# Kernel tuning notes

Measured on AMD Instinct MI355X. Metric: run time of the kernel, lower is better.

The kernel has to match this reference:

```python
import jax, jax.numpy as jnp
import numpy as np

K = 20
EPS_BN = 1e-5

def knn_idx(x, k):
    # x: [B,N,C] -> k nearest neighbor indices [B,N,k] (self included, as in DGCNN)
    sq = jnp.sum(x * x, axis=-1)                       # [B,N]
    inner = jnp.einsum('bnc,bmc->bnm', x, x)           # [B,N,N]
    neg_dist = 2.0 * inner - sq[:, :, None] - sq[:, None, :]
    _, idx = jax.lax.top_k(neg_dist, k)
    return jax.lax.stop_gradient(idx)

def edge_feat(x, idx):
    # x: [B,N,C], idx: [B,N,k] -> [B,N,k,2C] = cat([x_j - x_i, x_i])
    nbr = jax.vmap(lambda xb, ib: xb[ib])(x, idx)      # [B,N,k,C]
    ctr = jnp.broadcast_to(x[:, :, None, :], nbr.shape)
    return jnp.concatenate([nbr - ctr, ctr], axis=-1)

def edge_conv(x, W, g, b, k):
    e = edge_feat(x, knn_idx(x, k))                    # dynamic kNN graph per layer
    h = jnp.einsum('bnkc,cd->bnkd', e, W)              # 1x1 conv2d
    h = h * (g / jnp.sqrt(1.0 + EPS_BN)) + b           # BN eval (mean=0, var=1)
    return jnp.max(jax.nn.leaky_relu(h, 0.2), axis=2)  # max over neighbors -> [B,N,d]

def layer_norm(x, g, b):
    m = jnp.mean(x, axis=-1, keepdims=True)
    v = jnp.var(x, axis=-1, keepdims=True)
    return (x - m) * jax.lax.rsqrt(v + 1e-5) * g + b

def setup_inputs():
    key = jax.random.key(0)
    B, N = 2, 4096
    ks = jax.random.split(key, 16)
    w = lambda i, shape: jax.random.normal(ks[i], shape, jnp.float32) * 0.05
    ones = lambda d: jnp.ones((d,), jnp.float32)
    zeros = lambda d: jnp.zeros((d,), jnp.float32)
    return dict(
        xyz=jax.random.normal(ks[0], (N, 3), jnp.float32),
        scale=jax.random.normal(ks[1], (N, 3), jnp.float32),
        rot=jax.random.normal(ks[2], (N, 4), jnp.float32),
        opacity=jax.random.normal(ks[3], (N, 1), jnp.float32),
        color=jax.random.normal(ks[4], (N, 3), jnp.float32),
        pose=jax.random.normal(ks[5], (B, 75), jnp.float32),
        lbs_weights=jax.random.normal(ks[6], (N, 24), jnp.float32),
        Wc1=w(7, (226, 64)), g1=ones(64), b1=zeros(64),
        Wc2=w(8, (128, 64)), g2=ones(64), b2=zeros(64),
        Wc3=w(9, (128, 128)), g3=ones(128), b3=zeros(128),
        Wc4=w(10, (256, 256)), g4=ones(256), b4=zeros(256),
        Wc5=w(11, (512, 128)), g5=ones(128), b5=zeros(128),
        Wo1=w(12, (128, 128)), bo1=zeros(128), lg1=ones(128), lb1=zeros(128),
        Wo2=w(13, (128, 128)), bo2=zeros(128), lg2=ones(128), lb2=zeros(128),
        Wo3=w(14, (128, 38)), bo3=zeros(38),
    )

def reference(xyz, scale, rot, opacity, color, pose, lbs_weights,
              Wc1, g1, b1, Wc2, g2, b2, Wc3, g3, b3, Wc4, g4, b4, Wc5, g5, b5,
              Wo1, bo1, lg1, lb1, Wo2, bo2, lg2, lb2, Wo3, bo3):
    B, N = pose.shape[0], xyz.shape[0]
    gfeat = jnp.concatenate([xyz, scale, rot, opacity, color], axis=-1)   # [N,14]
    feats = jnp.concatenate([
        jnp.broadcast_to(gfeat[None], (B, N, gfeat.shape[-1])),
        jnp.broadcast_to(lbs_weights[None], (B, N, lbs_weights.shape[-1])),
        jnp.broadcast_to(pose[:, None, :], (B, N, pose.shape[-1])),
    ], axis=-1)                                                            # [B,N,113]
    # DGCNN graph encoder (dynamic kNN EdgeConv stack)
    x1 = edge_conv(feats, Wc1, g1, b1, K)   # [B,N,64]
    x2 = edge_conv(x1, Wc2, g2, b2, K)      # [B,N,64]
    x3 = edge_conv(x2, Wc3, g3, b3, K)      # [B,N,128]
    x4 = edge_conv(x3, Wc4, g4, b4, K)      # [B,N,256]
    cat = jnp.concatenate([x1, x2, x3, x4], axis=-1)                      # [B,N,512]
    gf = jax.nn.leaky_relu(
        jnp.einsum('bnc,cd->bnd', cat, Wc5) * (g5 / jnp.sqrt(1.0 + EPS_BN)) + b5, 0.2)
    # offset predictor MLP
    h = jax.nn.leaky_relu(layer_norm(gf @ Wo1 + bo1, lg1, lb1), 0.2)
    h = jax.nn.leaky_relu(layer_norm(h @ Wo2 + bo2, lg2, lb2), 0.2)
    off = h @ Wo3 + bo3                                                   # [B,N,38]
    # residual add of gaussian offsets (first 14 dims), lbs offsets raw (last 24)
    out = jnp.concatenate([gfeat[None] + off[..., :14], off[..., 14:]], axis=-1)
    return out                                                            # [B,N,38]
```

## Files before the change

kernel.cpp:

```cpp
#include <hip/hip_runtime.h>
#include <math.h>

#define KNN 20
#define BN_INV 0.9999950000374997f

__device__ __forceinline__ unsigned f2o(float f){
    unsigned u = __float_as_uint(f);
    return (u >> 31) ? ~u : (u | 0x80000000u);
}
__device__ __forceinline__ float o2f(unsigned u){
    return __uint_as_float((u >> 31) ? (u & 0x7fffffffu) : ~u);
}
__device__ __forceinline__ float leaky(float v){ return v > 0.f ? v : 0.2f * v; }

__global__ __launch_bounds__(128) void build_feats_kernel(
    const float* __restrict__ xyz, const float* __restrict__ scale,
    const float* __restrict__ rot, const float* __restrict__ opac,
    const float* __restrict__ color, const float* __restrict__ pose,
    const float* __restrict__ lbs, float* __restrict__ feats,
    float* __restrict__ sqout, int N)
{
    __shared__ float sred[2];
    int row = blockIdx.x;
    int b = row / N, n = row % N;
    int c = threadIdx.x;
    float v = 0.f;
    if      (c <   3) v = xyz  [n*3 + c];
    else if (c <   6) v = scale[n*3 + c-3];
    else if (c <  10) v = rot  [n*4 + c-6];
    else if (c <  11) v = opac [n];
    else if (c <  14) v = color[n*3 + c-11];
    else if (c <  38) v = lbs  [n*24 + c-14];
    else if (c < 113) v = pose [b*75 + c-38];
    if (c < 116) feats[(long)row*116 + c] = v;
    float ss = v * v;
    #pragma unroll
    for (int off = 32; off; off >>= 1) ss += __shfl_xor(ss, off);
    if ((c & 63) == 0) sred[c >> 6] = ss;
    __syncthreads();
    if (c == 0) sqout[row] = sred[0] + sred[1];
}


template<int C>
__global__ __launch_bounds__(256) void dist_gemm_kernel(
    const float* __restrict__ x, int N, int CP, float* __restrict__ G)
{
    __shared__ __align__(16) float smem[9216];
    float (*xi)[36] = (float(*)[36])smem;
    float (*xj)[36] = (float(*)[36])(smem + 128*36);

    const int q = blockIdx.x;
    int bjt = (int)((sqrtf(8.f*(float)q + 1.f) - 1.f) * 0.5f);
    while ((bjt+1)*(bjt+2)/2 <= q) ++bjt;
    while (bjt*(bjt+1)/2 > q) --bjt;
    const int bit = q - bjt*(bjt+1)/2;
    const int bi = bit * 128;
    const int bj = bjt * 128;

    const int b  = blockIdx.z;
    const int t  = threadIdx.x;
    const int tx = t & 15, ty = t >> 4;
    const int CP4 = CP / 4;
    const long base = (long)b * N;
    const float4* xp = (const float4*)x;

    float acc[8][8] = {};

    for (int c0 = 0; c0 < C; c0 += 32){
        const int KC  = (C - c0 < 32) ? (C - c0) : 32;
        const int KC4 = KC >> 2;
        __syncthreads();
        if (KC4 == 8){
            for (int f = t; f < 128 * 8; f += 256){
                int r = f >> 3, c4 = f & 7;
                *(float4*)&xi[r][c4 * 4] = xp[(base + bi + r) * CP4 + (c0 >> 2) + c4];
                *(float4*)&xj[r][c4 * 4] = xp[(base + bj + r) * CP4 + (c0 >> 2) + c4];
            }
        } else {
            for (int f = t; f < 128 * KC4; f += 256){
                int r = f / KC4, c4 = f - r * KC4;
                *(float4*)&xi[r][c4 * 4] = xp[(base + bi + r) * CP4 + (c0 >> 2) + c4];
                *(float4*)&xj[r][c4 * 4] = xp[(base + bj + r) * CP4 + (c0 >> 2) + c4];
            }
        }
        __syncthreads();
        for (int c = 0; c < KC; c += 4){
            float4 A[8], Bv[8];
            #pragma unroll
            for (int ii = 0; ii < 8; ++ii) A[ii]  = *(const float4*)&xi[ty + 16*ii][c];
            #pragma unroll
            for (int jj = 0; jj < 8; ++jj) Bv[jj] = *(const float4*)&xj[tx + 16*jj][c];
            #pragma unroll
            for (int ii = 0; ii < 8; ++ii)
                #pragma unroll
                for (int jj = 0; jj < 8; ++jj){
                    acc[ii][jj] = fmaf(A[ii].x, Bv[jj].x, acc[ii][jj]);
                    acc[ii][jj] = fmaf(A[ii].y, Bv[jj].y, acc[ii][jj]);
                    acc[ii][jj] = fmaf(A[ii].z, Bv[jj].z, acc[ii][jj]);
                    acc[ii][jj] = fmaf(A[ii].w, Bv[jj].w, acc[ii][jj]);
                }
        }
    }

    #pragma unroll
    for (int ii = 0; ii < 8; ++ii){
        long rbase = (base + bi + ty + 16*ii) * N + bj;
        #pragma unroll
        for (int jj = 0; jj < 8; ++jj)
            G[rbase + tx + 16*jj] = acc[ii][jj];
    }

    if (bi != bj){
        float (*tr)[132] = (float(*)[132])smem;
        #pragma unroll
        for (int h = 0; h < 2; ++h){
            __syncthreads();
            #pragma unroll
            for (int ii = 0; ii < 8; ++ii)
                #pragma unroll
                for (int jj = 4*h; jj < 4*h + 4; ++jj)
                    tr[tx + 16*(jj - 4*h)][ty + 16*ii] = acc[ii][jj];
            __syncthreads();
            const int cc = (t & 31) * 4;
            const int r0 = t >> 5;
            #pragma unroll
            for (int f = 0; f < 8; ++f){
                int r = r0 + 8 * f;
                *(float4*)&G[(base + bj + 64*h + r) * N + bi + cc] = *(const float4*)&tr[r][cc];
            }
        }
    }
}

#define TCAP 256
__global__ __launch_bounds__(256) void topk_kernel(
    const float* __restrict__ G, const float* __restrict__ sq,
    int N, int* __restrict__ idx_out)
{
    __shared__ unsigned smax[256];
    __shared__ unsigned cand_u[TCAP];
    __shared__ int      cand_j[TCAP];
    __shared__ unsigned cand_cnt;
    __shared__ unsigned sTu;

    const int row = blockIdx.x;
    const int b   = row >> 12;
    const int t   = threadIdx.x;
    const float4* g4  = (const float4*)(G  + (long)row * 4096);
    const float4* sq4 = (const float4*)(sq + (long)b   * 4096);

    unsigned u[16];
    #pragma unroll
    for (int qq = 0; qq < 4; ++qq){
        int v4 = t + 256 * qq;
        float4 gg = g4[v4];
        float4 ss = sq4[v4];
        u[4*qq+0] = f2o(fmaf(2.f, gg.x, -ss.x));
        u[4*qq+1] = f2o(fmaf(2.f, gg.y, -ss.y));
        u[4*qq+2] = f2o(fmaf(2.f, gg.z, -ss.z));
        u[4*qq+3] = f2o(fmaf(2.f, gg.w, -ss.w));
    }

    unsigned mu = u[0];
    #pragma unroll
    for (int q = 1; q < 16; ++q) mu = u[q] > mu ? u[q] : mu;
    smax[t] = mu;
    if (t == 0) cand_cnt = 0;
    __syncthreads();

    int rank = 0;
    for (int k = 0; k < 256; ++k){
        unsigned ou = smax[k];
        rank += (ou > mu) || (ou == mu && k < t);
    }
    if (rank == KNN - 1) sTu = mu;
    __syncthreads();
    const unsigned Tu = sTu;

    #pragma unroll
    for (int qq = 0; qq < 4; ++qq)
        #pragma unroll
        for (int m = 0; m < 4; ++m){
            int q = 4*qq + m;
            if (u[q] >= Tu){
                unsigned p = atomicAdd(&cand_cnt, 1u);
                if (p < TCAP){ cand_u[p] = u[q]; cand_j[p] = 4*(t + 256*qq) + m; }
            }
        }
    __syncthreads();
    const int cc = (int)cand_cnt;

    if (cc <= TCAP){
        if (t < cc){
            unsigned cu = cand_u[t]; int cj = cand_j[t];
            int r = 0;
            for (int k = 0; k < cc; ++k){
                unsigned ou = cand_u[k];
                r += (ou > cu) || (ou == cu && cand_j[k] < cj);
            }
            if (r < KNN) idx_out[(long)row * KNN + r] = cj;
        }
    } else {
        __shared__ unsigned rv[4]; __shared__ int ri[4]; __shared__ int gj_;
        unsigned lv = 0u; int lj = 0x7fffffff;
        #pragma unroll
        for (int q = 0; q < 16; ++q)
            if (u[q] > lv){ lv = u[q]; lj = 4*(t + 256*(q>>2)) + (q&3); }
        for (int it = 0; it < KNN; ++it){
            unsigned bv = lv; int bj = lj;
            #pragma unroll
            for (int off = 32; off; off >>= 1){
                unsigned ov = __shfl_xor(bv, off);
                int      oj = __shfl_xor(bj, off);
                if (ov > bv || (ov == bv && oj < bj)){ bv = ov; bj = oj; }
            }
            if ((t & 63) == 0){ rv[t >> 6] = bv; ri[t >> 6] = bj; }
            __syncthreads();
            if (t == 0){
                unsigned fv = rv[0]; int fj = ri[0];
                #pragma unroll
                for (int w = 1; w < 4; ++w)
                    if (rv[w] > fv || (rv[w] == fv && ri[w] < fj)){ fv = rv[w]; fj = ri[w]; }
                gj_ = fj;
                idx_out[(long)row * KNN + it] = fj;
            }
            __syncthreads();
            int fj = gj_;
            if (fj >= 0 && ((fj >> 2) & 255) == t){
                u[((fj >> 10) << 2) | (fj & 3)] = 0u;
                lv = 0u; lj = 0x7fffffff;
                #pragma unroll
                for (int q = 0; q < 16; ++q)
                    if (u[q] > lv){ lv = u[q]; lj = 4*(t + 256*(q>>2)) + (q&3); }
            }
            __syncthreads();
        }
    }
}


__device__ __forceinline__ void wcat_emit(const float* __restrict__ W, int C, int D,
                                          int i, float* __restrict__ dst)
{
    int TWOD = 2 * D;
    int c = i / TWOD, n = i - c * TWOD;
    float v = 0.f;
    if (c < C) v = (n < D) ? W[c*D + n] : (W[(C + c)*D + (n - D)] - W[c*D + (n - D)]);
    dst[i] = v;
}

__global__ void prep_all_wcat_kernel(
    const float* __restrict__ Wc1, const float* __restrict__ Wc2,
    const float* __restrict__ Wc3, const float* __restrict__ Wc4,
    float* __restrict__ Wcat)
{
    int i = blockIdx.x * 256 + threadIdx.x;
    if      (i <  14848) wcat_emit(Wc1, 113,  64, i,          Wcat);
    else if (i <  23040) wcat_emit(Wc2,  64,  64, i - 14848,  Wcat + 14848);
    else if (i <  39424) wcat_emit(Wc3,  64, 128, i - 23040,  Wcat + 23040);
    else if (i < 104960) wcat_emit(Wc4, 128, 256, i - 39424,  Wcat + 39424);
}

__global__ __launch_bounds__(256) void gemm_pq_kernel(
    const float* __restrict__ X, int CP, const float* __restrict__ Wcat,
    const float* __restrict__ g, const float* __restrict__ bias,
    int D, int TWOD, float* __restrict__ PQ)
{
    __shared__ __align__(16) float As[128][68];
    __shared__ __align__(16) float Bs[64][132];
    const int bi = blockIdx.x * 128;
    const int bn = blockIdx.y * 128;
    const int t  = threadIdx.x;
    const int tx = t & 15, ty = t >> 4;
    const int CP4 = CP / 4;
    const float4* xp = (const float4*)X;

    float acc[8][8] = {};

    for (int c0 = 0; c0 < CP; c0 += 64){
        const int KC = (CP - c0 < 64) ? (CP - c0) : 64;
        const int KC4 = KC >> 2;
        __syncthreads();
        for (int f = t; f < 128 * KC4; f += 256){
            int r = f / KC4, c4 = f - r * KC4;
            *(float4*)&As[r][c4 * 4] = xp[(long)(bi + r) * CP4 + (c0 >> 2) + c4];
        }
        for (int f = t; f < KC * 32; f += 256){
            int r = f >> 5, c4 = f & 31;
            *(float4*)&Bs[r][c4 * 4] = *(const float4*)&Wcat[(long)(c0 + r) * TWOD + bn + c4 * 4];
        }
        __syncthreads();
        for (int c = 0; c < KC; c += 4){
            float4 A[8];
            #pragma unroll
            for (int ii = 0; ii < 8; ++ii) A[ii] = *(const float4*)&As[ty + 16*ii][c];
            float Bv0[8], Bv1[8], Bv2[8], Bv3[8];
            #pragma unroll
            for (int jj = 0; jj < 8; ++jj){
                Bv0[jj] = Bs[c+0][tx + 16*jj];
                Bv1[jj] = Bs[c+1][tx + 16*jj];
                Bv2[jj] = Bs[c+2][tx + 16*jj];
                Bv3[jj] = Bs[c+3][tx + 16*jj];
            }
            #pragma unroll
            for (int ii = 0; ii < 8; ++ii)
                #pragma unroll
                for (int jj = 0; jj < 8; ++jj){
                    acc[ii][jj] = fmaf(A[ii].x, Bv0[jj], acc[ii][jj]);
                    acc[ii][jj] = fmaf(A[ii].y, Bv1[jj], acc[ii][jj]);
                    acc[ii][jj] = fmaf(A[ii].z, Bv2[jj], acc[ii][jj]);
                    acc[ii][jj] = fmaf(A[ii].w, Bv3[jj], acc[ii][jj]);
                }
        }
    }

    #pragma unroll
    for (int jj = 0; jj < 8; ++jj){
        int n = bn + tx + 16*jj;
        int d = (n < D) ? n : n - D;
        float gg = g[d] * BN_INV;
        float bb = (n < D) ? 0.f : bias[d];
        #pragma unroll
        for (int ii = 0; ii < 8; ++ii)
            PQ[(long)(bi + ty + 16*ii) * TWOD + n] = fmaf(acc[ii][jj], gg, bb);
    }
}

template<int D, int RPB>
__global__ __launch_bounds__(256) void gather_max_kernel(
    const float* __restrict__ PQ, const int* __restrict__ idx, int N,
    float* __restrict__ y, float* __restrict__ sqout)
{
    __shared__ int   lidx[RPB][KNN];
    __shared__ float sred[4];
    const int rb = blockIdx.x * RPB;
    const int t  = threadIdx.x;
    if (t < RPB * KNN) lidx[t / KNN][t % KNN] = idx[(long)rb * KNN + t];
    __syncthreads();

    const int r = t / D, d = t - r * D;
    const int row = rb + r;
    const long base = (long)(row / N) * N;
    const int TWOD = 2 * D;

    float q = PQ[(long)row * TWOD + D + d];
    float m = -INFINITY;
    #pragma unroll
    for (int k = 0; k < KNN; ++k){
        int j = lidx[r][k];
        m = fmaxf(m, PQ[(base + j) * TWOD + d]);
    }
    float val = leaky(m + q);
    y[(long)row * D + d] = val;

    float ss = val * val;
    #pragma unroll
    for (int off = 32; off; off >>= 1) ss += __shfl_xor(ss, off);
    if ((t & 63) == 0) sred[t >> 6] = ss;
    __syncthreads();
    if (d == 0){
        constexpr int WPR = D / 64;
        float s = 0.f;
        int w0 = (r * D) >> 6;
        #pragma unroll
        for (int w = 0; w < WPR; ++w) s += sred[w0 + w];
        sqout[row] = s;
    }
}

__global__ __launch_bounds__(256) void knn_kernel(
    const float* __restrict__ x, int N, int CP4, int* __restrict__ idx_out)
{
    __shared__ float4 xi4[32];
    __shared__ float drow[4096];
    __shared__ float rv[4];
    __shared__ int   ri[4];

    int row = blockIdx.x;
    int b = row / N;
    int t = threadIdx.x;
    const float4* xp = (const float4*)x;

    if (t < CP4) xi4[t] = xp[(long)row * CP4 + t];
    __syncthreads();

    long bb = (long)b * N * CP4;
    for (int j = t; j < N; j += 256){
        const float4* p = xp + bb + (long)j * CP4;
        float acc = 0.f;
        #pragma unroll 4
        for (int c = 0; c < CP4; ++c){
            float4 xv = p[c], yv = xi4[c];
            float dx = xv.x - yv.x, dy = xv.y - yv.y;
            float dz = xv.z - yv.z, dw = xv.w - yv.w;
            acc += dx*dx + dy*dy + dz*dz + dw*dw;
        }
        drow[j] = -acc;
    }
    __syncthreads();

    for (int it = 0; it < KNN; ++it){
        float bv = -INFINITY; int bi = N;
        for (int j = t; j < N; j += 256){
            float v = drow[j];
            if (v > bv){ bv = v; bi = j; }
        }
        #pragma unroll
        for (int off = 32; off > 0; off >>= 1){
            float ov = __shfl_xor(bv, off);
            int   oi = __shfl_xor(bi, off);
            if (ov > bv || (ov == bv && oi < bi)){ bv = ov; bi = oi; }
        }
        if ((t & 63) == 0){ rv[t >> 6] = bv; ri[t >> 6] = bi; }
        __syncthreads();
        if (t == 0){
            float fv = rv[0]; int fi = ri[0];
            #pragma unroll
            for (int w = 1; w < 4; ++w){
                if (rv[w] > fv || (rv[w] == fv && ri[w] < fi)){ fv = rv[w]; fi = ri[w]; }
            }
            idx_out[(long)row * KNN + it] = fi;
            drow[fi] = -INFINITY;
        }
        __syncthreads();
    }
}

template<int D, int KPT>
__global__ __launch_bounds__(256) void edge_conv_kernel(
    const float* __restrict__ x, int N, int C, int CP,
    const float* __restrict__ W, const float* __restrict__ g,
    const float* __restrict__ bias, const int* __restrict__ idx,
    float* __restrict__ y, float* __restrict__ sqout)
{
    __shared__ float xi[128];
    __shared__ float nbr[KNN * 128];
    __shared__ float t2[D];
    __shared__ unsigned um[D];
    __shared__ float sred[4];

    int row = blockIdx.x;
    int b = row / N;
    int t = threadIdx.x;

    for (int c = t; c < C; c += 256) xi[c] = x[(long)row * CP + c];
    for (int kk = 0; kk < KNN; ++kk){
        int j = idx[(long)row * KNN + kk];
        long nb = ((long)b * N + j) * CP;
        for (int c = t; c < C; c += 256) nbr[kk * C + c] = x[nb + c];
    }
    __syncthreads();

    for (int d = t; d < D; d += 256){
        float s = 0.f;
        for (int c = 0; c < C; ++c) s += xi[c] * W[(C + c) * D + d];
        t2[d] = s; um[d] = 0u;
    }
    __syncthreads();

    const int d  = t % D;
    const int kg = t / D;
    float s[KPT];
    #pragma unroll
    for (int q = 0; q < KPT; ++q) s[q] = t2[d];

    const float* nb0 = &nbr[(kg * KPT) * C];
    for (int c = 0; c < C; ++c){
        float w   = W[c * D + d];
        float xic = xi[c];
        #pragma unroll
        for (int q = 0; q < KPT; ++q)
            s[q] += (nb0[q * C + c] - xic) * w;
    }
    float g_ = g[d] * BN_INV, b_ = bias[d];
    float m = -INFINITY;
    #pragma unroll
    for (int q = 0; q < KPT; ++q)
        m = fmaxf(m, leaky(s[q] * g_ + b_));
    atomicMax(&um[d], f2o(m));
    __syncthreads();

    float ss = 0.f;
    for (int dd = t; dd < D; dd += 256){
        float val = o2f(um[dd]);
        y[(long)row * D + dd] = val;
        ss += val * val;
    }
    #pragma unroll
    for (int off = 32; off; off >>= 1) ss += __shfl_xor(ss, off);
    if ((t & 63) == 0) sred[t >> 6] = ss;
    __syncthreads();
    if (t == 0) sqout[row] = sred[0] + sred[1] + sred[2] + sred[3];
}

#define HP 8
__global__ __launch_bounds__(128) void head_kernel(
    const float* __restrict__ x1, const float* __restrict__ x2,
    const float* __restrict__ x3, const float* __restrict__ x4,
    const float* __restrict__ feats,
    const float* __restrict__ Wc5, const float* __restrict__ g5, const float* __restrict__ b5,
    const float* __restrict__ Wo1, const float* __restrict__ bo1,
    const float* __restrict__ lg1, const float* __restrict__ lb1,
    const float* __restrict__ Wo2, const float* __restrict__ bo2,
    const float* __restrict__ lg2, const float* __restrict__ lb2,
    const float* __restrict__ Wo3, const float* __restrict__ bo3,
    float* __restrict__ out, int N, int R)
{
    __shared__ __align__(16) float cat[HP][520];
    __shared__ __align__(16) float hb[HP][132];
    __shared__ float wsum[2][HP], wsq[2][HP];
    __shared__ float f14[HP][14];

    const int t = threadIdx.x;
    const long p0 = (long)blockIdx.x * HP;
    const int wid = t >> 6;

    long rows[HP];
    #pragma unroll
    for (int p = 0; p < HP; ++p){
        long row = p0 + p; if (row >= R) row = R - 1;
        rows[p] = row;
        cat[p][t]       = (t < 64) ? x1[row*64 + t] : x2[row*64 + (t-64)];
        cat[p][128 + t] = x3[row*128 + t];
        cat[p][256 + t] = x4[row*256 + t];
        cat[p][384 + t] = x4[row*256 + 128 + t];
        if (t < 14) f14[p][t] = feats[row*116 + t];
    }
    __syncthreads();

    const float g5t = g5[t] * BN_INV, b5t = b5[t];
    float acc[HP];
    #pragma unroll
    for (int p = 0; p < HP; ++p) acc[p] = 0.f;
    for (int c4 = 0; c4 < 128; ++c4){
        float w0 = Wc5[(4*c4+0)*128 + t];
        float w1 = Wc5[(4*c4+1)*128 + t];
        float w2 = Wc5[(4*c4+2)*128 + t];
        float w3 = Wc5[(4*c4+3)*128 + t];
        #pragma unroll
        for (int p = 0; p < HP; ++p){
            float4 cv = *(const float4*)&cat[p][4*c4];
            acc[p] = fmaf(cv.x, w0, acc[p]);
            acc[p] = fmaf(cv.y, w1, acc[p]);
            acc[p] = fmaf(cv.z, w2, acc[p]);
            acc[p] = fmaf(cv.w, w3, acc[p]);
        }
    }
    #pragma unroll
    for (int p = 0; p < HP; ++p) hb[p][t] = leaky(fmaf(acc[p], g5t, b5t));
    __syncthreads();

    for (int layer = 0; layer < 2; ++layer){
        const float* W  = layer ? Wo2 : Wo1;
        const float* bo = layer ? bo2 : bo1;
        const float* lg = layer ? lg2 : lg1;
        const float* lb = layer ? lb2 : lb1;
        float a2[HP];
        float bot = bo[t];
        #pragma unroll
        for (int p = 0; p < HP; ++p) a2[p] = bot;
        for (int c4 = 0; c4 < 32; ++c4){
            float w0 = W[(4*c4+0)*128 + t];
            float w1 = W[(4*c4+1)*128 + t];
            float w2 = W[(4*c4+2)*128 + t];
            float w3 = W[(4*c4+3)*128 + t];
            #pragma unroll
            for (int p = 0; p < HP; ++p){
                float4 hv = *(const float4*)&hb[p][4*c4];
                a2[p] = fmaf(hv.x, w0, a2[p]);
                a2[p] = fmaf(hv.y, w1, a2[p]);
                a2[p] = fmaf(hv.z, w2, a2[p]);
                a2[p] = fmaf(hv.w, w3, a2[p]);
            }
        }
        #pragma unroll
        for (int p = 0; p < HP; ++p){
            float s1 = a2[p], s2 = a2[p]*a2[p];
            #pragma unroll
            for (int off = 32; off; off >>= 1){
                s1 += __shfl_xor(s1, off);
                s2 += __shfl_xor(s2, off);
            }
            if ((t & 63) == 0){ wsum[wid][p] = s1; wsq[wid][p] = s2; }
        }
        __syncthreads();
        float lgt = lg[t], lbt = lb[t];
        float hn[HP];
        #pragma unroll
        for (int p = 0; p < HP; ++p){
            float m  = (wsum[0][p] + wsum[1][p]) * (1.f/128.f);
            float v  = (wsq[0][p]  + wsq[1][p])  * (1.f/128.f) - m*m;
            float dm = a2[p] - m;
            hn[p] = leaky(dm * rsqrtf(v + 1e-5f) * lgt + lbt);
        }
        __syncthreads();
        #pragma unroll
        for (int p = 0; p < HP; ++p) hb[p][t] = hn[p];
        __syncthreads();
    }

    if (t < 38){
        float o[HP];
        float bt = bo3[t];
        #pragma unroll
        for (int p = 0; p < HP; ++p) o[p] = bt;
        for (int c = 0; c < 128; ++c){
            float w = Wo3[c*38 + t];
            #pragma unroll
            for (int p = 0; p < HP; ++p) o[p] = fmaf(hb[p][c], w, o[p]);
        }
        #pragma unroll
        for (int p = 0; p < HP; ++p){
            float val = o[p] + ((t < 14) ? f14[p][t] : 0.f);
            out[rows[p]*38 + t] = val;
        }
    }
}

extern "C" void kernel_launch(void* const* d_in, const int* in_sizes, int n_in,
                              void* d_out, int out_size, void* d_ws, size_t ws_size,
                              hipStream_t stream)
{
    const float* xyz  = (const float*)d_in[0];
    const float* scal = (const float*)d_in[1];
    const float* rot  = (const float*)d_in[2];
    const float* opac = (const float*)d_in[3];
    const float* colr = (const float*)d_in[4];
    const float* pose = (const float*)d_in[5];
    const float* lbs  = (const float*)d_in[6];
    const float* Wc1 = (const float*)d_in[7];  const float* g1 = (const float*)d_in[8];  const float* b1 = (const float*)d_in[9];
    const float* Wc2 = (const float*)d_in[10]; const float* g2 = (const float*)d_in[11]; const float* b2 = (const float*)d_in[12];
    const float* Wc3 = (const float*)d_in[13]; const float* g3 = (const float*)d_in[14]; const float* b3 = (const float*)d_in[15];
    const float* Wc4 = (const float*)d_in[16]; const float* g4 = (const float*)d_in[17]; const float* b4 = (const float*)d_in[18];
    const float* Wc5 = (const float*)d_in[19]; const float* g5 = (const float*)d_in[20]; const float* b5 = (const float*)d_in[21];
    const float* Wo1 = (const float*)d_in[22]; const float* bo1 = (const float*)d_in[23];
    const float* lg1 = (const float*)d_in[24]; const float* lb1 = (const float*)d_in[25];
    const float* Wo2 = (const float*)d_in[26]; const float* bo2 = (const float*)d_in[27];
    const float* lg2 = (const float*)d_in[28]; const float* lb2 = (const float*)d_in[29];
    const float* Wo3 = (const float*)d_in[30]; const float* bo3 = (const float*)d_in[31];

    const int N = in_sizes[0] / 3;
    const int B = in_sizes[5] / 75;
    const int R = B * N;

    char* ws = (char*)d_ws;
    size_t o = 0;
    float* feats = (float*)(ws + o); o += (size_t)R * 116 * 4;
    float* x1    = (float*)(ws + o); o += (size_t)R * 64  * 4;
    float* x2    = (float*)(ws + o); o += (size_t)R * 64  * 4;
    float* x3    = (float*)(ws + o); o += (size_t)R * 128 * 4;
    float* x4    = (float*)(ws + o); o += (size_t)R * 256 * 4;
    int*   idx   = (int*)  (ws + o); o += (size_t)R * KNN * 4;
    float* sq    = (float*)(ws + o); o += (size_t)R * 4;
    float* Wcat  = (float*)(ws + o); o += (size_t)104960 * 4;
    float* G     = (float*)(ws + o);
    float* PQ    = G;
    size_t need  = o + (size_t)B * N * N * 4;

    const bool fast = (N == 4096) && (ws_size >= need);

    build_feats_kernel<<<R, 128, 0, stream>>>(xyz, scal, rot, opac, colr, pose, lbs, feats, sq, N);

    if (fast){
        const int NT = 32;
        dim3 gg(NT*(NT+1)/2, 1, B);
        float* Wcat1 = Wcat;
        float* Wcat2 = Wcat + 14848;
        float* Wcat3 = Wcat + 23040;
        float* Wcat4 = Wcat + 39424;

        prep_all_wcat_kernel<<<(104960 + 255)/256, 256, 0, stream>>>(Wc1, Wc2, Wc3, Wc4, Wcat);

        dist_gemm_kernel<116><<<gg, 256, 0, stream>>>(feats, N, 116, G);
        topk_kernel<<<R, 256, 0, stream>>>(G, sq, N, idx);
        gemm_pq_kernel<<<dim3(R/128, 1), 256, 0, stream>>>(feats, 116, Wcat1, g1, b1, 64, 128, PQ);
        gather_max_kernel<64, 4><<<R/4, 256, 0, stream>>>(PQ, idx, N, x1, sq);

        dist_gemm_kernel<64><<<gg, 256, 0, stream>>>(x1, N, 64, G);
        topk_kernel<<<R, 256, 0, stream>>>(G, sq, N, idx);
        gemm_pq_kernel<<<dim3(R/128, 1), 256, 0, stream>>>(x1, 64, Wcat2, g2, b2, 64, 128, PQ);
        gather_max_kernel<64, 4><<<R/4, 256, 0, stream>>>(PQ, idx, N, x2, sq);

        dist_gemm_kernel<64><<<gg, 256, 0, stream>>>(x2, N, 64, G);
        topk_kernel<<<R, 256, 0, stream>>>(G, sq, N, idx);
        gemm_pq_kernel<<<dim3(R/128, 2), 256, 0, stream>>>(x2, 64, Wcat3, g3, b3, 128, 256, PQ);
        gather_max_kernel<128, 2><<<R/2, 256, 0, stream>>>(PQ, idx, N, x3, sq);

        dist_gemm_kernel<128><<<gg, 256, 0, stream>>>(x3, N, 128, G);
        topk_kernel<<<R, 256, 0, stream>>>(G, sq, N, idx);
        gemm_pq_kernel<<<dim3(R/128, 4), 256, 0, stream>>>(x3, 128, Wcat4, g4, b4, 256, 512, PQ);
        gather_max_kernel<256, 1><<<R, 256, 0, stream>>>(PQ, idx, N, x4, sq);
    } else {
        knn_kernel<<<R, 256, 0, stream>>>(feats, N, 116/4, idx);
        edge_conv_kernel<64, 5><<<R, 256, 0, stream>>>(feats, N, 113, 116, Wc1, g1, b1, idx, x1, sq);
        knn_kernel<<<R, 256, 0, stream>>>(x1, N, 64/4, idx);
        edge_conv_kernel<64, 5><<<R, 256, 0, stream>>>(x1, N, 64, 64, Wc2, g2, b2, idx, x2, sq);
        knn_kernel<<<R, 256, 0, stream>>>(x2, N, 64/4, idx);
        edge_conv_kernel<128, 10><<<R, 256, 0, stream>>>(x2, N, 64, 64, Wc3, g3, b3, idx, x3, sq);
        knn_kernel<<<R, 256, 0, stream>>>(x3, N, 128/4, idx);
        edge_conv_kernel<256, 20><<<R, 256, 0, stream>>>(x3, N, 128, 128, Wc4, g4, b4, idx, x4, sq);
    }

    head_kernel<<<(R + HP - 1)/HP, 128, 0, stream>>>(x1, x2, x3, x4, feats,
                                       Wc5, g5, b5, Wo1, bo1, lg1, lb1,
                                       Wo2, bo2, lg2, lb2, Wo3, bo3,
                                       (float*)d_out, N, R);
}
```

Measured before the change: 842.3 us.

## Split head MLP into tiled shared-memory GEMM kernels on fast path

On the fast path, the single per-point head kernel is replaced by four kernels. A 64x64-tiled SGEMM computes the 512->128 projection with BN and leaky ReLU. Two tiled GEMMs fuse layer norm and leaky ReLU for the 128x128 layers, and a small kernel produces the 38-wide output plus the residual. The goal is better weight reuse through shared-memory tiling instead of per-point weight streaming. The cost is three extra launches and intermediate buffers round-tripping through global memory (aliased onto the G workspace).

```diff
diff --git a/kernel.cpp b/kernel.cpp
--- a/kernel.cpp
+++ b/kernel.cpp
@@ -366,6 +366,188 @@
         #pragma unroll
         for (int w = 0; w < WPR; ++w) s += sred[w0 + w];
         sqout[row] = s;
+    }
+}
+
+
+__global__ __launch_bounds__(256) void head_gemm1_kernel(
+    const float* __restrict__ x1, const float* __restrict__ x2,
+    const float* __restrict__ x3, const float* __restrict__ x4,
+    const float* __restrict__ Wc5, const float* __restrict__ g5,
+    const float* __restrict__ b5, float* __restrict__ gf, int R)
+{
+    __shared__ __align__(16) float As[64][68];
+    __shared__ __align__(16) float Bs[64][68];
+    const int bi = blockIdx.x * 64;
+    const int bn = blockIdx.y * 64;
+    const int t  = threadIdx.x;
+    const int tx = t & 15, ty = t >> 4;
+
+    float acc[4][4] = {};
+
+    #pragma unroll 1
+    for (int kc = 0; kc < 8; ++kc){
+        const float* src; int ld, coff;
+        if      (kc == 0){ src = x1; ld = 64;  coff = 0; }
+        else if (kc == 1){ src = x2; ld = 64;  coff = 0; }
+        else if (kc <  4){ src = x3; ld = 128; coff = (kc-2)*64; }
+        else             { src = x4; ld = 256; coff = (kc-4)*64; }
+        __syncthreads();
+        for (int f = t; f < 64*16; f += 256){
+            int r = f >> 4, c4 = f & 15;
+            *(float4*)&As[r][c4*4] = *(const float4*)&src[(long)(bi + r)*ld + coff + c4*4];
+            *(float4*)&Bs[r][c4*4] = *(const float4*)&Wc5[(long)(kc*64 + r)*128 + bn + c4*4];
+        }
+        __syncthreads();
+        for (int c = 0; c < 64; c += 4){
+            float4 A[4];
+            #pragma unroll
+            for (int ii = 0; ii < 4; ++ii) A[ii] = *(const float4*)&As[ty + 16*ii][c];
+            float B0[4], B1[4], B2[4], B3[4];
+            #pragma unroll
+            for (int jj = 0; jj < 4; ++jj){
+                B0[jj] = Bs[c+0][tx + 16*jj];
+                B1[jj] = Bs[c+1][tx + 16*jj];
+                B2[jj] = Bs[c+2][tx + 16*jj];
+                B3[jj] = Bs[c+3][tx + 16*jj];
+            }
+            #pragma unroll
+            for (int ii = 0; ii < 4; ++ii)
+                #pragma unroll
+                for (int jj = 0; jj < 4; ++jj){
+                    acc[ii][jj] = fmaf(A[ii].x, B0[jj], acc[ii][jj]);
+                    acc[ii][jj] = fmaf(A[ii].y, B1[jj], acc[ii][jj]);
+                    acc[ii][jj] = fmaf(A[ii].z, B2[jj], acc[ii][jj]);
+                    acc[ii][jj] = fmaf(A[ii].w, B3[jj], acc[ii][jj]);
+                }
+        }
+    }
+
+    #pragma unroll
+    for (int jj = 0; jj < 4; ++jj){
+        int n = bn + tx + 16*jj;
+        float gg = g5[n] * BN_INV, bb = b5[n];
+        #pragma unroll
+        for (int ii = 0; ii < 4; ++ii)
+            gf[(long)(bi + ty + 16*ii)*128 + n] = leaky(fmaf(acc[ii][jj], gg, bb));
+    }
+}
+
+__global__ __launch_bounds__(256) void head_lngemm_kernel(
+    const float* __restrict__ hin, const float* __restrict__ W,
+    const float* __restrict__ bo, const float* __restrict__ lg,
+    const float* __restrict__ lb, float* __restrict__ hout, int R)
+{
+    __shared__ __align__(16) float As[64][68];
+    __shared__ __align__(16) float Bs[64][132];
+    const int bi = blockIdx.x * 64;
+    const int t  = threadIdx.x;
+    const int tx = t & 15, ty = t >> 4;
+
+    float acc[4][8] = {};
+
+    #pragma unroll 1
+    for (int kc = 0; kc < 2; ++kc){
+        __syncthreads();
+        for (int f = t; f < 64*16; f += 256){
+            int r = f >> 4, c4 = f & 15;
+            *(float4*)&As[r][c4*4] = *(const float4*)&hin[(long)(bi + r)*128 + kc*64 + c4*4];
+        }
+        for (int f = t; f < 64*32; f += 256){
+            int r = f >> 5, c4 = f & 31;
+            *(float4*)&Bs[r][c4*4] = *(const float4*)&W[(long)(kc*64 + r)*128 + c4*4];
+        }
+        __syncthreads();
+        for (int c = 0; c < 64; c += 4){
+            float4 A[4];
+            #pragma unroll
+            for (int ii = 0; ii < 4; ++ii) A[ii] = *(const float4*)&As[ty + 16*ii][c];
+            float B0[8], B1[8], B2[8], B3[8];
+            #pragma unroll
+            for (int jj = 0; jj < 8; ++jj){
+                B0[jj] = Bs[c+0][tx + 16*jj];
+                B1[jj] = Bs[c+1][tx + 16*jj];
+                B2[jj] = Bs[c+2][tx + 16*jj];
+                B3[jj] = Bs[c+3][tx + 16*jj];
+            }
+            #pragma unroll
+            for (int ii = 0; ii < 4; ++ii)
+                #pragma unroll
+                for (int jj = 0; jj < 8; ++jj){
+                    acc[ii][jj] = fmaf(A[ii].x, B0[jj], acc[ii][jj]);
+                    acc[ii][jj] = fmaf(A[ii].y, B1[jj], acc[ii][jj]);
+                    acc[ii][jj] = fmaf(A[ii].z, B2[jj], acc[ii][jj]);
+                    acc[ii][jj] = fmaf(A[ii].w, B3[jj], acc[ii][jj]);
+                }
+        }
+    }
+
+    float bon[8], lgn[8], lbn[8];
+    #pragma unroll
+    for (int jj = 0; jj < 8; ++jj){
+        int n = tx + 16*jj;
+        bon[jj] = bo[n]; lgn[jj] = lg[n]; lbn[jj] = lb[n];
+    }
+    #pragma unroll
+    for (int ii = 0; ii < 4; ++ii){
+        float s1 = 0.f, s2 = 0.f;
+        #pragma unroll
+        for (int jj = 0; jj < 8; ++jj){
+            float a = acc[ii][jj] + bon[jj];
+            acc[ii][jj] = a;
+            s1 += a; s2 += a*a;
+        }
+        #pragma unroll
+        for (int off = 8; off; off >>= 1){
+            s1 += __shfl_xor(s1, off);
+            s2 += __shfl_xor(s2, off);
+        }
+        float m = s1 * (1.f/128.f);
+        float v = s2 * (1.f/128.f) - m*m;
+        float rinv = rsqrtf(v + 1e-5f);
+        long r = bi + ty + 16*ii;
+        #pragma unroll
+        for (int jj = 0; jj < 8; ++jj)
+            hout[r*128 + tx + 16*jj] = leaky((acc[ii][jj] - m) * rinv * lgn[jj] + lbn[jj]);
+    }
+}
+
+#define OP 16
+__global__ __launch_bounds__(256) void head_out_kernel(
+    const float* __restrict__ h, const float* __restrict__ feats,
+    const float* __restrict__ Wo3, const float* __restrict__ bo3,
+    float* __restrict__ out, int R)
+{
+    __shared__ __align__(16) float hs[OP][132];
+    __shared__ float f14[OP][14];
+    const int t  = threadIdx.x;
+    const long p0 = (long)blockIdx.x * OP;
+
+    for (int f = t; f < OP*32; f += 256){
+        int r = f >> 5, c4 = f & 31;
+        *(float4*)&hs[r][c4*4] = *(const float4*)&h[(p0 + r)*128 + c4*4];
+    }
+    if (t < OP*14) f14[t/14][t%14] = feats[(p0 + t/14)*116 + t%14];
+    __syncthreads();
+
+    const int w = t >> 6, l = t & 63;
+    if (l < 38){
+        float o[4];
+        float bt = bo3[l];
+        #pragma unroll
+        for (int pp = 0; pp < 4; ++pp) o[pp] = bt;
+        for (int c = 0; c < 128; ++c){
+            float wv = Wo3[c*38 + l];
+            #pragma unroll
+            for (int pp = 0; pp < 4; ++pp)
+                o[pp] = fmaf(hs[w*4 + pp][c], wv, o[pp]);
+        }
+        #pragma unroll
+        for (int pp = 0; pp < 4; ++pp){
+            int p = w*4 + pp;
+            float val = o[pp] + ((l < 14) ? f14[p][l] : 0.f);
+            out[(p0 + p)*38 + l] = val;
+        }
     }
 }
 
@@ -656,6 +838,9 @@
     float* Wcat  = (float*)(ws + o); o += (size_t)104960 * 4;
     float* G     = (float*)(ws + o);
     float* PQ    = G;
+    float* gf    = G;
+    float* h1    = G + (size_t)R * 128;
+    float* h2    = G + (size_t)R * 256;
     size_t need  = o + (size_t)B * N * N * 4;
 
     const bool fast = (N == 4096) && (ws_size >= need);
@@ -691,6 +876,11 @@
         topk_kernel<<<R, 256, 0, stream>>>(G, sq, N, idx);
         gemm_pq_kernel<<<dim3(R/128, 4), 256, 0, stream>>>(x3, 128, Wcat4, g4, b4, 256, 512, PQ);
         gather_max_kernel<256, 1><<<R, 256, 0, stream>>>(PQ, idx, N, x4, sq);
+
+        head_gemm1_kernel<<<dim3(R/64, 2), 256, 0, stream>>>(x1, x2, x3, x4, Wc5, g5, b5, gf, R);
+        head_lngemm_kernel<<<R/64, 256, 0, stream>>>(gf, Wo1, bo1, lg1, lb1, h1, R);
+        head_lngemm_kernel<<<R/64, 256, 0, stream>>>(h1, Wo2, bo2, lg2, lb2, h2, R);
+        head_out_kernel<<<R/OP, 256, 0, stream>>>(h2, feats, Wo3, bo3, (float*)d_out, R);
     } else {
         knn_kernel<<<R, 256, 0, stream>>>(feats, N, 116/4, idx);
         edge_conv_kernel<64, 5><<<R, 256, 0, stream>>>(feats, N, 113, 116, Wc1, g1, b1, idx, x1, sq);
@@ -700,10 +890,10 @@
         edge_conv_kernel<128, 10><<<R, 256, 0, stream>>>(x2, N, 64, 64, Wc3, g3, b3, idx, x3, sq);
         knn_kernel<<<R, 256, 0, stream>>>(x3, N, 128/4, idx);
         edge_conv_kernel<256, 20><<<R, 256, 0, stream>>>(x3, N, 128, 128, Wc4, g4, b4, idx, x4, sq);
-    }
-
-    head_kernel<<<(R + HP - 1)/HP, 128, 0, stream>>>(x1, x2, x3, x4, feats,
-                                       Wc5, g5, b5, Wo1, bo1, lg1, lb1,
-                                       Wo2, bo2, lg2, lb2, Wo3, bo3,
-                                       (float*)d_out, N, R);
-}
+
+        head_kernel<<<(R + HP - 1)/HP, 128, 0, stream>>>(x1, x2, x3, x4, feats,
+                                           Wc5, g5, b5, Wo1, bo1, lg1, lb1,
+                                           Wo2, bo2, lg2, lb2, Wo3, bo3,
+                                           (float*)d_out, N, R);
+    }
+}
```

Measured after the change: 832.4 us. Within noise of the previous version (-1.2%).
